# Kernel optimization log

Measured on AMD Instinct MI355X. Metric: run time of the kernel, lower is better.

## Reference

```python
import jax, jax.numpy as jnp
import numpy as np

NUM_BASES = 8
DEGREE = 3
KSIZE = 3
DOMAIN = (0.0, 1.0)


def bspline_basis(x, degree, knots):
    """Cox-de Boor recursion, vectorized over all elements of x.
    x: [...] float; knots: [num_bases + degree + 1].
    Returns basis values of shape [..., num_bases].
    (The original torch code evaluates this same recursion per-tap inside
    nested loops; here it is evaluated once, batched, with correct knot
    index bookkeeping. Uniform distinct knots -> no zero denominators.)
    """
    xe = x[..., None]  # [..., 1]
    # degree-0: indicator of each knot interval -> [..., L-1]
    B = ((knots[:-1] <= xe) & (xe < knots[1:])).astype(x.dtype)
    for d in range(1, degree + 1):
        left = (xe - knots[:-(d + 1)]) / (knots[d:-1] - knots[:-(d + 1)]) * B[..., :-1]
        right = (knots[d + 1:] - xe) / (knots[d + 1:] - knots[1:-d]) * B[..., 1:]
        B = left + right  # [..., L-d-1]
    return B  # [..., num_bases]


def setup_inputs() -> dict:
    key = jax.random.key(0)
    k1, k2 = jax.random.split(key)
    # inputs uniform in [0,1) so they lie inside the B-spline domain
    x = jax.random.uniform(k1, (16, 64, 64, 64), dtype=jnp.float32)
    # per-tap spline coefficients: [Cout, Cin, K, K, num_bases]
    coeff = jax.random.normal(k2, (64, 64, KSIZE, KSIZE, NUM_BASES), dtype=jnp.float32)
    return {"x": x, "coeff": coeff}


def reference(x, coeff):
    # normalize to domain (identity for domain=(0,1), kept for faithfulness)
    xn = (x - DOMAIN[0]) / (DOMAIN[1] - DOMAIN[0])
    knots = jnp.linspace(DOMAIN[0], DOMAIN[1], NUM_BASES + DEGREE + 1, dtype=x.dtype)
    # spline basis for every input element: [B, Cin, H, W, nb]
    phi = bspline_basis(xn, DEGREE, knots)
    Bn, Cin, H, W, nb = phi.shape
    Cout = coeff.shape[0]
    # The KAN conv  out[b,o,h,w] = sum_{j,k,l,m} phi[b,j,h+k,w+l,m]*coeff[o,j,k,l,m]
    # is exactly a VALID conv with Cin*nb input channels.
    phi_c = jnp.transpose(phi, (0, 1, 4, 2, 3)).reshape(Bn, Cin * nb, H, W)
    w = jnp.transpose(coeff, (0, 1, 4, 2, 3)).reshape(Cout, Cin * nb, KSIZE, KSIZE)
    out = jax.lax.conv_general_dilated(
        phi_c, w, window_strides=(1, 1), padding="VALID",
        dimension_numbers=("NCHW", "OIHW", "NCHW"))
    return out  # [B, Cout, H-K+1, W-K+1]
```

## Files before the change

### kernel.cpp

```cpp
#include <hip/hip_runtime.h>
#include <hip/hip_bf16.h>


typedef short v8s __attribute__((ext_vector_type(8)));
typedef float v4f __attribute__((ext_vector_type(4)));
typedef float v16f __attribute__((ext_vector_type(16)));
typedef unsigned long long u64;
typedef u64 v2u64 __attribute__((ext_vector_type(2)));

#define B_N   16
#define CIN   64
#define COUT  64
#define H_IN  64
#define W_IN  64
#define NB    8
#define HO    62
#define WO    62
#define JC    8
#define NCH   8

__device__ __forceinline__ ushort f2bf(float f) {
    uint xu = __float_as_uint(f);
    return (ushort)((xu + 0x7fffu + ((xu >> 16) & 1u)) >> 16);
}

__device__ __forceinline__ uint cvtpk(float a, float b) {
    uint r;
    asm("v_cvt_pk_bf16_f32 %0, %1, %2" : "=v"(r) : "v"(a), "v"(b));
    return r;
}

__global__ void prep_coeff_kernel(const float* __restrict__ coeff, ushort* __restrict__ bt) {
    int n = blockIdx.x * 256 + threadIdx.x;
    if (n >= 294912) return;
    int m  = n & 7;
    int g2 = (n >> 3) & 1;
    int o  = (n >> 4) & 63;
    int jp = (n >> 10) & 3;
    int q  = n >> 12;
    int tap = q % 9;
    int jc  = q / 9;
    int j = jc * 8 + jp * 2 + g2;
    bt[n] = f2bf(coeff[((o * CIN + j) * 9 + tap) * 8 + m]);
}

#define MFMA32(a, b, c) __builtin_amdgcn_mfma_f32_32x32x16_bf16((a), (b), (c), 0, 0, 0)
#define MFMA16(a, b, c) __builtin_amdgcn_mfma_f32_16x16x32_bf16((a), (b), (c), 0, 0, 0)

__global__ __launch_bounds__(256, 4) void kan_conv_pf(
        const float* __restrict__ x, const ushort* __restrict__ cb,
        float* __restrict__ out) {
    const int h    = blockIdx.x;
    const int b    = blockIdx.y;
    const int tid  = threadIdx.x;
    const int lane = tid & 63;
    const int kh   = tid >> 6;
    const int l31  = lane & 31;
    const int g2   = lane >> 5;

    __shared__ __align__(16) char smraw[32768];

    char* wrB = smraw + kh * 6144 + lane * 16;
    const char* rdB = smraw + kh * 6144 + g2 * 1024 + l31 * 16;

    v16f acc[2][2];
    acc[0][0] = (v16f)(0.f); acc[0][1] = (v16f)(0.f);
    acc[1][0] = (v16f)(0.f); acc[1][1] = (v16f)(0.f);

    float xr[6];
    const float* xb = x + ((size_t)(b * CIN) * H_IN + h) * W_IN + lane;
    const int jx = kh * 2;

#define XL(dst, jcn) { \
    _Pragma("unroll") \
    for (int e = 0; e < 6; ++e) \
        dst[e] = xb[(size_t)((jcn) * 8 + jx + (e & 1)) * (H_IN * W_IN) + (e >> 1) * W_IN]; \
    }

    auto PW = [&](float xval, int e) {
        float s_ = fminf(fmaxf(xval * 11.0f, 0.0f), 10.999f);
        int i0 = (int)s_;
        float u  = s_ - (float)i0;
        float t  = 1.0f - u;
        float u2 = u * u, u3 = u2 * u;
        float t3 = t * t * t;
        const float inv6 = 1.0f / 6.0f;
        float n0 = t3 * inv6;
        float n3 = u3 * inv6;
        float n1 = fmaf(u2, fmaf(u, 0.5f, -1.0f), 2.0f / 3.0f);
        float n2 = 1.0f - n0 - n1 - n3;
        u64 V = (u64)cvtpk(n0, n1) | ((u64)cvtpk(n2, n3) << 32);
        int bi = i0 - 3;
        u64 lo = bi < 0 ? (V >> (uint)(-16 * bi))
               : bi < 4 ? (V << (uint)(16 * bi)) : 0ull;
        u64 hi = bi <= 0 ? 0ull
               : bi < 4 ? (V >> (uint)(64 - 16 * bi))
               : (V << (uint)(16 * bi - 64));
        v2u64 pk; pk[0] = lo; pk[1] = hi;
        *reinterpret_cast<v2u64*>(wrB + e * 1024) = pk;
    };

    const char* pA = (const char*)cb + (size_t)(kh * 128 + l31 * 2 + g2) * 16;

    v8s a0A, a1A, a0B, a1B, a0C, a1C;

#define TAPR(k, lt, C0, C1, N0, N1, nptr) { \
    v8s b0 = *reinterpret_cast<const v8s*>(rdB + (k) * 2048 + (lt) * 16); \
    v8s b1 = *reinterpret_cast<const v8s*>(rdB + (k) * 2048 + 512 + (lt) * 16); \
    N0 = *reinterpret_cast<const v8s*>(nptr); \
    N1 = *reinterpret_cast<const v8s*>((nptr) + 1024); \
    acc[0][0] = MFMA32(C0, b0, acc[0][0]); \
    acc[0][1] = MFMA32(C0, b1, acc[0][1]); \
    acc[1][0] = MFMA32(C1, b0, acc[1][0]); \
    acc[1][1] = MFMA32(C1, b1, acc[1][1]); }

#define CHUNKP(jc) { \
    const char* pAc = pA + (size_t)(jc) * 73728; \
    const char* pAn = pA + (size_t)(((jc) + 1 < NCH) ? (jc) + 1 : 0) * 73728; \
    if ((jc) + 1 < NCH) XL(xr, (jc) + 1); \
    TAPR(0, 0, a0A, a1A, a0C, a1C, pAc + 2 * 8192); \
    TAPR(0, 1, a0B, a1B, a0A, a1A, pAc + 3 * 8192); \
    TAPR(0, 2, a0C, a1C, a0B, a1B, pAc + 4 * 8192); \
    if ((jc) + 1 < NCH) { PW(xr[0], 0); PW(xr[1], 1); } \
    TAPR(1, 0, a0A, a1A, a0C, a1C, pAc + 5 * 8192); \
    TAPR(1, 1, a0B, a1B, a0A, a1A, pAc + 6 * 8192); \
    TAPR(1, 2, a0C, a1C, a0B, a1B, pAc + 7 * 8192); \
    if ((jc) + 1 < NCH) { PW(xr[2], 2); PW(xr[3], 3); } \
    TAPR(2, 0, a0A, a1A, a0C, a1C, pAc + 8 * 8192); \
    TAPR(2, 1, a0B, a1B, a0A, a1A, pAn + 0 * 8192); \
    TAPR(2, 2, a0C, a1C, a0B, a1B, pAn + 1 * 8192); \
    if ((jc) + 1 < NCH) { PW(xr[4], 4); PW(xr[5], 5); } \
    }

    XL(xr, 0);
    PW(xr[0], 0); PW(xr[1], 1); PW(xr[2], 2);
    PW(xr[3], 3); PW(xr[4], 4); PW(xr[5], 5);
    a0A = *reinterpret_cast<const v8s*>(pA);
    a1A = *reinterpret_cast<const v8s*>(pA + 1024);
    a0B = *reinterpret_cast<const v8s*>(pA + 8192);
    a1B = *reinterpret_cast<const v8s*>(pA + 8192 + 1024);

    CHUNKP(0); CHUNKP(1); CHUNKP(2); CHUNKP(3);
    CHUNKP(4); CHUNKP(5); CHUNKP(6); CHUNKP(7);

#define WR_FULL(off) { \
    _Pragma("unroll") \
    for (int t = 0; t < 4; ++t) { \
        _Pragma("unroll") \
        for (int q = 0; q < 4; ++q) { \
            v4f v; \
            _Pragma("unroll") \
            for (int z = 0; z < 4; ++z) v[z] = acc[t >> 1][t & 1][q * 4 + z]; \
            *reinterpret_cast<v4f*>(smraw + (off) + (t * 4 + q) * 1024 + lane * 16) = v; \
        } } }
#define ADD_FULL(off) { \
    _Pragma("unroll") \
    for (int t = 0; t < 4; ++t) { \
        _Pragma("unroll") \
        for (int q = 0; q < 4; ++q) { \
            v4f v = *reinterpret_cast<const v4f*>(smraw + (off) + (t * 4 + q) * 1024 + lane * 16); \
            _Pragma("unroll") \
            for (int z = 0; z < 4; ++z) acc[t >> 1][t & 1][q * 4 + z] += v[z]; \
        } } }
#define WR_HALF(OT, off) { \
    _Pragma("unroll") \
    for (int wf = 0; wf < 2; ++wf) { \
        _Pragma("unroll") \
        for (int q = 0; q < 4; ++q) { \
            v4f v; \
            _Pragma("unroll") \
            for (int z = 0; z < 4; ++z) v[z] = acc[OT][wf][q * 4 + z]; \
            *reinterpret_cast<v4f*>(smraw + (off) + (wf * 4 + q) * 1024 + lane * 16) = v; \
        } } }
#define ADD_HALF(OT, off) { \
    _Pragma("unroll") \
    for (int wf = 0; wf < 2; ++wf) { \
        _Pragma("unroll") \
        for (int q = 0; q < 4; ++q) { \
            v4f v = *reinterpret_cast<const v4f*>(smraw + (off) + (wf * 4 + q) * 1024 + lane * 16); \
            _Pragma("unroll") \
            for (int z = 0; z < 4; ++z) acc[OT][wf][q * 4 + z] += v[z]; \
        } } }
#define STORE_HALF(OT) { \
    _Pragma("unroll") \
    for (int wf = 0; wf < 2; ++wf) { \
        int w = wf * 32 + l31; \
        if (w < WO) { \
            _Pragma("unroll") \
            for (int reg = 0; reg < 16; ++reg) { \
                int o = (OT) * 32 + (reg & 3) + 8 * (reg >> 2) + 4 * g2; \
                out[((b * COUT + o) * HO + h) * WO + w] = acc[OT][wf][reg]; \
            } } } }

    __syncthreads();
    if (kh == 1) WR_FULL(0);
    if (kh == 3) WR_FULL(16384);
    __syncthreads();
    if (kh == 0) ADD_FULL(0);
    if (kh == 2) ADD_FULL(16384);
    __syncthreads();
    if (kh == 2) WR_HALF(0, 0);
    if (kh == 0) WR_HALF(1, 8192);
    __syncthreads();
    if (kh == 0) { ADD_HALF(0, 0);    STORE_HALF(0); }
    if (kh == 2) { ADD_HALF(1, 8192); STORE_HALF(1); }
}

__global__ __launch_bounds__(256, 4) void kan_conv_fb(
        const float* __restrict__ x, const float* __restrict__ coeff_f,
        float* __restrict__ out) {
    const int h    = blockIdx.x;
    const int b    = blockIdx.y;
    const int tid  = threadIdx.x;
    const int lane = tid & 63;
    const int wv   = tid >> 6;
    const int g    = lane >> 4;
    const int l15  = lane & 15;
    const int obase = (wv >> 1) << 5;
    const int wbase = (wv & 1) << 5;

    __shared__ __align__(16) ushort phi_lds[3 * JC * W_IN * NB];
    __shared__ uint lut[72];
    if (tid < 72) {
        int tap = tid;
        int j  = tap / 9;
        int r9 = tap - j * 9;
        int kt = r9 / 3;
        int lt = r9 - kt * 3;
        lut[tap] = (uint)(((kt * JC + j) * W_IN) * NB) | ((uint)lt << 16)
                 | ((uint)j << 20) | ((uint)r9 << 24);
    }
    v4f acc00 = {0.f, 0.f, 0.f, 0.f};
    v4f acc01 = acc00, acc10 = acc00, acc11 = acc00;
    const int aoff = obase + l15;
    float xv[6];
    #pragma unroll
    for (int it = 0; it < 6; ++it) {
        int n = it * 256 + tid;
        xv[it] = x[((b * CIN + ((n >> 6) & 7)) * H_IN + (h + (n >> 9))) * W_IN + (n & 63)];
    }
    for (int jc = 0; jc < NCH; ++jc) {
        #pragma unroll
        for (int it = 0; it < 6; ++it) {
            int n = it * 256 + tid;
            float s  = xv[it] * 11.0f;
            int i0 = (int)s;
            i0 = i0 < 0 ? 0 : (i0 > 10 ? 10 : i0);
            float u  = s - (float)i0;
            float um = 1.0f - u;
            float u2 = u * u, u3 = u2 * u;
            const float inv6 = 1.0f / 6.0f;
            float n0 = um * um * um * inv6;
            float n1 = (3.0f * u3 - 6.0f * u2 + 4.0f) * inv6;
            float n2 = (-3.0f * u3 + 3.0f * u2 + 3.0f * u + 1.0f) * inv6;
            float n3 = u3 * inv6;
            u64 V = (u64)f2bf(n0) | ((u64)f2bf(n1) << 16)
                  | ((u64)f2bf(n2) << 32) | ((u64)f2bf(n3) << 48);
            int bi = i0 - 3;
            u64 lo = bi < 0 ? (V >> (uint)(-16 * bi))
                   : bi < 4 ? (V << (uint)(16 * bi)) : 0ull;
            u64 hi = bi <= 0 ? 0ull
                   : bi < 4 ? (V >> (uint)(64 - 16 * bi))
                   : (V << (uint)(16 * bi - 64));
            v2u64 pk; pk[0] = lo; pk[1] = hi;
            *reinterpret_cast<v2u64*>(&phi_lds[n << 3]) = pk;
        }
        if (jc + 1 < NCH) {
            int j0n = (jc + 1) * JC;
            #pragma unroll
            for (int it = 0; it < 6; ++it) {
                int n = it * 256 + tid;
                xv[it] = x[((b * CIN + j0n + ((n >> 6) & 7)) * H_IN + (h + (n >> 9))) * W_IN + (n & 63)];
            }
        }
        __syncthreads();
        const int j0 = jc * JC;
        #pragma unroll 6
        for (int kk = 0; kk < 18; ++kk) {
            int tap = (kk << 2) + g;
            uint e = lut[tap];
            int philoc = (int)(e & 0xffffu);
            int lt     = (int)((e >> 16) & 3u);
            int w0 = wbase + l15 + lt;
            int w1 = w0 + 16;
            w0 = w0 < 63 ? w0 : 63;
            w1 = w1 < 63 ? w1 : 63;
            v8s pb0 = *reinterpret_cast<const v8s*>(&phi_lds[philoc + (w0 << 3)]);
            v8s pb1 = *reinterpret_cast<const v8s*>(&phi_lds[philoc + (w1 << 3)]);
            int j  = (int)((e >> 20) & 15u);
            int r9 = (int)((e >> 24) & 15u);
            const float* cf = coeff_f + (((aoff * CIN + (j0 + j)) * 9 + r9) << 3);
            v8s pa0, pa1;
            #pragma unroll
            for (int z = 0; z < 8; ++z) pa0[z] = (short)f2bf(cf[z]);
            const float* cf2 = cf + (CIN * 9 * NB * 16);
            #pragma unroll
            for (int z = 0; z < 8; ++z) pa1[z] = (short)f2bf(cf2[z]);
            acc00 = MFMA16(pa0, pb0, acc00);
            acc01 = MFMA16(pa0, pb1, acc01);
            acc10 = MFMA16(pa1, pb0, acc10);
            acc11 = MFMA16(pa1, pb1, acc11);
        }
        __syncthreads();
    }
    const int wc0 = wbase + l15;
    const int wc1 = wc0 + 16;
    #pragma unroll
    for (int i = 0; i < 2; ++i) {
        v4f a0 = (i == 0) ? acc00 : acc10;
        v4f a1 = (i == 0) ? acc01 : acc11;
        int o = obase + i * 16 + (g << 2);
        #pragma unroll
        for (int r = 0; r < 4; ++r) {
            int off = ((b * COUT + o + r) * HO + h) * WO;
            if (wc0 < WO) out[off + wc0] = a0[r];
            if (wc1 < WO) out[off + wc1] = a1[r];
        }
    }
}

extern "C" void kernel_launch(void* const* d_in, const int* in_sizes, int n_in,
                              void* d_out, int out_size, void* d_ws, size_t ws_size,
                              hipStream_t stream) {
    const float* x     = (const float*)d_in[0];
    const float* coeff = (const float*)d_in[1];
    float* out = (float*)d_out;

    const size_t bt_bytes = (size_t)294912 * 2;
    if (ws_size >= bt_bytes) {
        ushort* bt = (ushort*)d_ws;
        prep_coeff_kernel<<<(294912 + 255) / 256, 256, 0, stream>>>(coeff, bt);
        kan_conv_pf<<<dim3(HO, B_N), 256, 0, stream>>>(x, bt, out);
    } else {
        kan_conv_fb<<<dim3(HO, B_N), 256, 0, stream>>>(x, coeff, out);
    }
}
```

Baseline: 52.67 us.

## Split output channels across two blocks per row to raise occupancy

```diff
diff --git a/kernel.cpp b/kernel.cpp
--- a/kernel.cpp
+++ b/kernel.cpp
@@ -47,25 +47,24 @@
 #define MFMA32(a, b, c) __builtin_amdgcn_mfma_f32_32x32x16_bf16((a), (b), (c), 0, 0, 0)
 #define MFMA16(a, b, c) __builtin_amdgcn_mfma_f32_16x16x32_bf16((a), (b), (c), 0, 0, 0)
 
-__global__ __launch_bounds__(256, 4) void kan_conv_pf(
+__global__ __launch_bounds__(256, 5) void kan_conv_os(
         const float* __restrict__ x, const ushort* __restrict__ cb,
         float* __restrict__ out) {
     const int h    = blockIdx.x;
     const int b    = blockIdx.y;
+    const int obh  = blockIdx.z;
     const int tid  = threadIdx.x;
     const int lane = tid & 63;
     const int kh   = tid >> 6;
     const int l31  = lane & 31;
     const int g2   = lane >> 5;
 
-    __shared__ __align__(16) char smraw[32768];
+    __shared__ __align__(16) char smraw[24576];
 
     char* wrB = smraw + kh * 6144 + lane * 16;
     const char* rdB = smraw + kh * 6144 + g2 * 1024 + l31 * 16;
 
-    v16f acc[2][2];
-    acc[0][0] = (v16f)(0.f); acc[0][1] = (v16f)(0.f);
-    acc[1][0] = (v16f)(0.f); acc[1][1] = (v16f)(0.f);
+    v16f c0 = (v16f)(0.f), c1 = (v16f)(0.f);
 
     float xr[6];
     const float* xb = x + ((size_t)(b * CIN) * H_IN + h) * W_IN + lane;
@@ -100,110 +99,80 @@
         *reinterpret_cast<v2u64*>(wrB + e * 1024) = pk;
     };
 
-    const char* pA = (const char*)cb + (size_t)(kh * 128 + l31 * 2 + g2) * 16;
-
-    v8s a0A, a1A, a0B, a1B, a0C, a1C;
-
-#define TAPR(k, lt, C0, C1, N0, N1, nptr) { \
+    const char* pA = (const char*)cb + (size_t)(kh * 128 + obh * 64 + l31 * 2 + g2) * 16;
+
+    v8s aA, aB, aC;
+
+#define TAPR(k, lt, C, N, nptr) { \
     v8s b0 = *reinterpret_cast<const v8s*>(rdB + (k) * 2048 + (lt) * 16); \
     v8s b1 = *reinterpret_cast<const v8s*>(rdB + (k) * 2048 + 512 + (lt) * 16); \
-    N0 = *reinterpret_cast<const v8s*>(nptr); \
-    N1 = *reinterpret_cast<const v8s*>((nptr) + 1024); \
-    acc[0][0] = MFMA32(C0, b0, acc[0][0]); \
-    acc[0][1] = MFMA32(C0, b1, acc[0][1]); \
-    acc[1][0] = MFMA32(C1, b0, acc[1][0]); \
-    acc[1][1] = MFMA32(C1, b1, acc[1][1]); }
+    N = *reinterpret_cast<const v8s*>(nptr); \
+    c0 = MFMA32(C, b0, c0); \
+    c1 = MFMA32(C, b1, c1); }
 
 #define CHUNKP(jc) { \
     const char* pAc = pA + (size_t)(jc) * 73728; \
     const char* pAn = pA + (size_t)(((jc) + 1 < NCH) ? (jc) + 1 : 0) * 73728; \
     if ((jc) + 1 < NCH) XL(xr, (jc) + 1); \
-    TAPR(0, 0, a0A, a1A, a0C, a1C, pAc + 2 * 8192); \
-    TAPR(0, 1, a0B, a1B, a0A, a1A, pAc + 3 * 8192); \
-    TAPR(0, 2, a0C, a1C, a0B, a1B, pAc + 4 * 8192); \
+    TAPR(0, 0, aA, aC, pAc + 2 * 8192); \
+    TAPR(0, 1, aB, aA, pAc + 3 * 8192); \
+    TAPR(0, 2, aC, aB, pAc + 4 * 8192); \
     if ((jc) + 1 < NCH) { PW(xr[0], 0); PW(xr[1], 1); } \
-    TAPR(1, 0, a0A, a1A, a0C, a1C, pAc + 5 * 8192); \
-    TAPR(1, 1, a0B, a1B, a0A, a1A, pAc + 6 * 8192); \
-    TAPR(1, 2, a0C, a1C, a0B, a1B, pAc + 7 * 8192); \
+    TAPR(1, 0, aA, aC, pAc + 5 * 8192); \
+    TAPR(1, 1, aB, aA, pAc + 6 * 8192); \
+    TAPR(1, 2, aC, aB, pAc + 7 * 8192); \
     if ((jc) + 1 < NCH) { PW(xr[2], 2); PW(xr[3], 3); } \
-    TAPR(2, 0, a0A, a1A, a0C, a1C, pAc + 8 * 8192); \
-    TAPR(2, 1, a0B, a1B, a0A, a1A, pAn + 0 * 8192); \
-    TAPR(2, 2, a0C, a1C, a0B, a1B, pAn + 1 * 8192); \
+    TAPR(2, 0, aA, aC, pAc + 8 * 8192); \
+    TAPR(2, 1, aB, aA, pAn + 0 * 8192); \
+    TAPR(2, 2, aC, aB, pAn + 1 * 8192); \
     if ((jc) + 1 < NCH) { PW(xr[4], 4); PW(xr[5], 5); } \
     }
 
     XL(xr, 0);
+    aA = *reinterpret_cast<const v8s*>(pA);
+    aB = *reinterpret_cast<const v8s*>(pA + 8192);
     PW(xr[0], 0); PW(xr[1], 1); PW(xr[2], 2);
     PW(xr[3], 3); PW(xr[4], 4); PW(xr[5], 5);
-    a0A = *reinterpret_cast<const v8s*>(pA);
-    a1A = *reinterpret_cast<const v8s*>(pA + 1024);
-    a0B = *reinterpret_cast<const v8s*>(pA + 8192);
-    a1B = *reinterpret_cast<const v8s*>(pA + 8192 + 1024);
 
     CHUNKP(0); CHUNKP(1); CHUNKP(2); CHUNKP(3);
     CHUNKP(4); CHUNKP(5); CHUNKP(6); CHUNKP(7);
 
-#define WR_FULL(off) { \
+#define WR1(C, off) { \
     _Pragma("unroll") \
-    for (int t = 0; t < 4; ++t) { \
+    for (int q = 0; q < 4; ++q) { \
+        v4f v; \
         _Pragma("unroll") \
-        for (int q = 0; q < 4; ++q) { \
-            v4f v; \
-            _Pragma("unroll") \
-            for (int z = 0; z < 4; ++z) v[z] = acc[t >> 1][t & 1][q * 4 + z]; \
-            *reinterpret_cast<v4f*>(smraw + (off) + (t * 4 + q) * 1024 + lane * 16) = v; \
+        for (int z = 0; z < 4; ++z) v[z] = C[q * 4 + z]; \
+        *reinterpret_cast<v4f*>(smraw + (off) + q * 1024 + lane * 16) = v; \
+    } }
+#define ADD1(C, off) { \
+    _Pragma("unroll") \
+    for (int q = 0; q < 4; ++q) { \
+        v4f v = *reinterpret_cast<const v4f*>(smraw + (off) + q * 1024 + lane * 16); \
+        _Pragma("unroll") \
+        for (int z = 0; z < 4; ++z) C[q * 4 + z] += v[z]; \
+    } }
+#define STORE1(C, WF) { \
+    int w = (WF) * 32 + l31; \
+    if (w < WO) { \
+        _Pragma("unroll") \
+        for (int reg = 0; reg < 16; ++reg) { \
+            int o = obh * 32 + (reg & 3) + 8 * (reg >> 2) + 4 * g2; \
+            out[((b * COUT + o) * HO + h) * WO + w] = C[reg]; \
         } } }
-#define ADD_FULL(off) { \
-    _Pragma("unroll") \
-    for (int t = 0; t < 4; ++t) { \
-        _Pragma("unroll") \
-        for (int q = 0; q < 4; ++q) { \
-            v4f v = *reinterpret_cast<const v4f*>(smraw + (off) + (t * 4 + q) * 1024 + lane * 16); \
-            _Pragma("unroll") \
-            for (int z = 0; z < 4; ++z) acc[t >> 1][t & 1][q * 4 + z] += v[z]; \
-        } } }
-#define WR_HALF(OT, off) { \
-    _Pragma("unroll") \
-    for (int wf = 0; wf < 2; ++wf) { \
-        _Pragma("unroll") \
-        for (int q = 0; q < 4; ++q) { \
-            v4f v; \
-            _Pragma("unroll") \
-            for (int z = 0; z < 4; ++z) v[z] = acc[OT][wf][q * 4 + z]; \
-            *reinterpret_cast<v4f*>(smraw + (off) + (wf * 4 + q) * 1024 + lane * 16) = v; \
-        } } }
-#define ADD_HALF(OT, off) { \
-    _Pragma("unroll") \
-    for (int wf = 0; wf < 2; ++wf) { \
-        _Pragma("unroll") \
-        for (int q = 0; q < 4; ++q) { \
-            v4f v = *reinterpret_cast<const v4f*>(smraw + (off) + (wf * 4 + q) * 1024 + lane * 16); \
-            _Pragma("unroll") \
-            for (int z = 0; z < 4; ++z) acc[OT][wf][q * 4 + z] += v[z]; \
-        } } }
-#define STORE_HALF(OT) { \
-    _Pragma("unroll") \
-    for (int wf = 0; wf < 2; ++wf) { \
-        int w = wf * 32 + l31; \
-        if (w < WO) { \
-            _Pragma("unroll") \
-            for (int reg = 0; reg < 16; ++reg) { \
-                int o = (OT) * 32 + (reg & 3) + 8 * (reg >> 2) + 4 * g2; \
-                out[((b * COUT + o) * HO + h) * WO + w] = acc[OT][wf][reg]; \
-            } } } }
 
     __syncthreads();
-    if (kh == 1) WR_FULL(0);
-    if (kh == 3) WR_FULL(16384);
+    if (kh == 1) { WR1(c0, 0);     WR1(c1, 4096); }
+    if (kh == 3) { WR1(c0, 8192);  WR1(c1, 12288); }
     __syncthreads();
-    if (kh == 0) ADD_FULL(0);
-    if (kh == 2) ADD_FULL(16384);
+    if (kh == 0) { ADD1(c0, 0);    ADD1(c1, 4096); }
+    if (kh == 2) { ADD1(c0, 8192); ADD1(c1, 12288); }
     __syncthreads();
-    if (kh == 2) WR_HALF(0, 0);
-    if (kh == 0) WR_HALF(1, 8192);
+    if (kh == 2) WR1(c0, 16384);
+    if (kh == 0) WR1(c1, 20480);
     __syncthreads();
-    if (kh == 0) { ADD_HALF(0, 0);    STORE_HALF(0); }
-    if (kh == 2) { ADD_HALF(1, 8192); STORE_HALF(1); }
+    if (kh == 0) { ADD1(c0, 16384); STORE1(c0, 0); }
+    if (kh == 2) { ADD1(c1, 20480); STORE1(c1, 1); }
 }
 
 __global__ __launch_bounds__(256, 4) void kan_conv_fb(
@@ -330,7 +299,7 @@
     if (ws_size >= bt_bytes) {
         ushort* bt = (ushort*)d_ws;
         prep_coeff_kernel<<<(294912 + 255) / 256, 256, 0, stream>>>(coeff, bt);
-        kan_conv_pf<<<dim3(HO, B_N), 256, 0, stream>>>(x, bt, out);
+        kan_conv_os<<<dim3(HO, B_N, 2), 256, 0, stream>>>(x, bt, out);
     } else {
         kan_conv_fb<<<dim3(HO, B_N), 256, 0, stream>>>(x, coeff, out);
     }
```

Measured after the change: 59.42 us. +12.8%, slower.
